# Performance work log

Hardware: AMD Instinct MI355X
Metric: run time of the kernel (lower is better)

## Reference

```python
import jax, jax.numpy as jnp
import numpy as np

N_KV, GROUP, D = 8, 4, 128
N_HEADS = N_KV * GROUP  # 32
B = 16
CONTEXT = 32768
S_CACHE = 32640  # pad = CONTEXT - B - S_CACHE = 112
NEG_INF = -10000.0


def setup_inputs() -> dict:
    key = jax.random.key(0)
    ks = jax.random.split(key, 5)
    queries = jax.random.normal(ks[0], (N_HEADS, B, D), jnp.float32)
    keys = jax.random.normal(ks[1], (N_KV, B, D), jnp.float32)
    key_t_caches = jax.random.normal(ks[2], (N_KV, D, S_CACHE), jnp.float32)
    values = jax.random.normal(ks[3], (N_KV, B, D), jnp.float32)
    value_caches = jax.random.normal(ks[4], (N_KV, S_CACHE, D), jnp.float32)
    # causal + padding mask bias: cache positions fully visible; new token j
    # sees new tokens 0..j; padded tail (and future new tokens) masked.
    pos = jnp.arange(CONTEXT)  # [context]
    new_idx = pos - S_CACHE
    qidx = jnp.arange(B)[:, None]  # [B,1]
    valid = (pos[None, :] < S_CACHE) | ((new_idx[None, :] >= 0) & (new_idx[None, :] <= qidx) & (new_idx[None, :] < B))
    attn_bias = jnp.where(valid, 0.0, NEG_INF).astype(jnp.float32)  # [B, context]
    kq_scale = jnp.float32(1.0 / np.sqrt(D))
    return {"queries": queries, "keys": keys, "key_t_caches": key_t_caches,
            "values": values, "value_caches": value_caches,
            "attn_bias": attn_bias, "kq_scale": kq_scale}


def reference(queries, keys, key_t_caches, values, value_caches, attn_bias, kq_scale):
    n_kv, d, s_cache = key_t_caches.shape
    n_heads, b, _ = queries.shape
    group = n_heads // n_kv
    context = attn_bias.shape[-1]
    pad = context - b - s_cache

    scaled_keys = keys * kq_scale                      # [n_kv, B, D]
    scaled_values = jnp.maximum(values, NEG_INF)       # [n_kv, B, D]

    key_t = jnp.swapaxes(scaled_keys, 1, 2)            # [n_kv, D, B]
    padded_key_t = jnp.pad(key_t, ((0, 0), (0, 0), (0, pad)))
    all_keys_t = jnp.concatenate([key_t_caches, padded_key_t], axis=-1)   # [n_kv, D, context]

    padded_values = jnp.pad(scaled_values, ((0, 0), (0, pad), (0, 0)))
    all_values = jnp.concatenate([value_caches, padded_values], axis=1)   # [n_kv, context, D]

    q = queries.reshape(n_kv, group, b, d)             # grouped queries per kv head
    scores = jnp.einsum('kgbd,kdc->kgbc', q, all_keys_t) + attn_bias      # [n_kv, g, B, context]
    probs = jax.nn.softmax(scores, axis=-1)
    out = jnp.einsum('kgbc,kcd->kgbd', probs, all_values)                 # [n_kv, g, B, D]
    # torch.cat(head_outs, dim=-1): head order = kv*group + g
    out = jnp.transpose(out, (2, 0, 1, 3)).reshape(b, n_heads * d)        # [B, n_heads*D]
    return out, scaled_keys, scaled_values
```

## Files before the change

### kernel.cpp

```cpp
#include <hip/hip_runtime.h>
#include <hip/hip_bf16.h>

#define NKV 8
#define GROUP 4
#define NH 32
#define BQ 16
#define DH 128
#define SC 32640
#define CTX 32768
#define SVALID (SC + BQ)
#define NEGB (-10000.0f)
#define CH2 128
#define KST 136
#define VST 68
#define PST 72
#define SPLIT_BYTES 266240ull

typedef short bf16x4 __attribute__((ext_vector_type(4)));
typedef short bf16x8 __attribute__((ext_vector_type(8)));
typedef float f32x4 __attribute__((ext_vector_type(4)));

static __device__ __forceinline__ short f2bf(float f) {
  __hip_bfloat16 h = __float2bfloat16(f);
  short s; __builtin_memcpy(&s, &h, sizeof(s));
  return s;
}
static __device__ __forceinline__ unsigned pack2(float lo, float hi) {
  return ((unsigned)(unsigned short)f2bf(lo)) | (((unsigned)(unsigned short)f2bf(hi)) << 16);
}

__global__ __launch_bounds__(256, 2)
void attn_partial(const float* __restrict__ q,
                  const float* __restrict__ keys,
                  const float* __restrict__ ktc,
                  const float* __restrict__ values,
                  const float* __restrict__ vc,
                  const float* __restrict__ kq_scale_p,
                  float* __restrict__ ws_acc,
                  float* __restrict__ ws_ml,
                  int splen)
{
  __shared__ __align__(16) short k_sh[128 * KST];
  __shared__ __align__(16) short v_sh[2][128 * VST];
  __shared__ __align__(16) short p_sh[4][16 * PST];

  const int kv    = blockIdx.y;
  const int split = blockIdx.x;
  const int tid   = threadIdx.x;
  const int wid   = tid >> 6;
  const int lane  = tid & 63;
  const int l15   = lane & 15;
  const int l4    = lane >> 4;
  const int hg    = kv * GROUP + wid;
  const float kscale = *kq_scale_p;

  bf16x8 qb[4];
  {
    const float* qrow = q + ((size_t)hg * BQ + l15) * DH + l4 * 8;
    #pragma unroll
    for (int kk = 0; kk < 4; ++kk) {
      #pragma unroll
      for (int j = 0; j < 8; ++j) qb[kk][j] = f2bf(qrow[kk * 32 + j]);
    }
  }

  float m_run = -3.0e38f, l_run = 0.f;
  f32x4 acc[8];
  #pragma unroll
  for (int n = 0; n < 8; ++n) acc[n] = (f32x4){0.f, 0.f, 0.f, 0.f};

  const int c_begin = split * splen;
  int c_end      = c_begin + splen; if (c_end > SVALID) c_end = SVALID;
  int staged_end = c_begin + splen; if (staged_end > SC) staged_end = SC;
  const int nch  = (staged_end - c_begin) >> 7;

  float4 kregL[8], kregH[8], vreg[16];

  auto load_k = [&](int cc) {
    const float* kp = ktc + (size_t)kv * DH * SC + cc;
    #pragma unroll
    for (int p = 0; p < 8; ++p) {
      const int d = p * 16 + (tid >> 4);
      const float* row = kp + (size_t)d * SC + (tid & 15) * 4;
      kregL[p] = *reinterpret_cast<const float4*>(row);
      kregH[p] = *reinterpret_cast<const float4*>(row + 64);
    }
  };
  auto load_v = [&](int cc) {
    const float* vp = vc + ((size_t)kv * SC + cc) * DH;
    #pragma unroll
    for (int p = 0; p < 16; ++p) {
      const int c = p * 8 + (tid >> 5);
      vreg[p] = *reinterpret_cast<const float4*>(vp + (size_t)c * DH + (tid & 31) * 4);
    }
  };
  auto store_k_half = [&](float4 (&kr)[8], int h) {
    const int u  = tid & 15;
    const int r  = (tid >> 4) & 3;
    const int wv = tid >> 6;
    #pragma unroll
    for (int p = 0; p < 8; ++p) {
      float x[4] = {kr[p].x, kr[p].y, kr[p].z, kr[p].w};
      float x2[4], y[4];
      #pragma unroll
      for (int c = 0; c < 4; ++c) {
        float s = __shfl_xor(x[c ^ 1], 16);
        x2[c] = ((c ^ r) & 1) ? s : x[c];
      }
      #pragma unroll
      for (int c = 0; c < 4; ++c) {
        float s = __shfl_xor(x2[c ^ 2], 32);
        y[c] = ((c ^ r) & 2) ? s : x2[c];
      }
      bf16x4 wk;
      #pragma unroll
      for (int j = 0; j < 4; ++j) wk[j] = f2bf(y[j]);
      *reinterpret_cast<bf16x4*>(&k_sh[(h * 64 + 4 * u + r) * KST + p * 16 + 4 * wv]) = wk;
    }
  };
  auto store_v = [&]() {
    const int b5 = (tid >> 5) & 1;
    #pragma unroll
    for (int p = 0; p < 16; ++p) {
      short* vs = v_sh[p >> 3];
      const float v0 = vreg[p].x, v1 = vreg[p].y, v2 = vreg[p].z, v3 = vreg[p].w;
      const float s0 = b5 ? v0 : v2;
      const float s1 = b5 ? v1 : v3;
      const float r0 = __shfl_xor(s0, 32);
      const float r1 = __shfl_xor(s1, 32);
      const float lo0 = b5 ? r0 : v0, hi0 = b5 ? v2 : r0;
      const float lo1 = b5 ? r1 : v1, hi1 = b5 ? v3 : r1;
      const int db = 4 * (tid & 31) + 2 * b5;
      const int c0 = (p & 7) * 8 + ((tid >> 5) & ~1);
      *reinterpret_cast<unsigned*>(&vs[(db + 0) * VST + c0]) = pack2(lo0, hi0);
      *reinterpret_cast<unsigned*>(&vs[(db + 1) * VST + c0]) = pack2(lo1, hi1);
    }
  };

  auto compute_half = [&](int h) {
    f32x4 s4[4];
    #pragma unroll
    for (int t = 0; t < 4; ++t) {
      f32x4 cacc = {0.f, 0.f, 0.f, 0.f};
      #pragma unroll
      for (int kk = 0; kk < 4; ++kk) {
        const bf16x8 ka = *reinterpret_cast<const bf16x8*>(
            &k_sh[(h * 64 + t * 16 + l15) * KST + kk * 32 + l4 * 8]);
        cacc = __builtin_amdgcn_mfma_f32_16x16x32_bf16(ka, qb[kk], cacc, 0, 0, 0);
      }
      s4[t] = cacc;
    }

    float mx = s4[0][0];
    #pragma unroll
    for (int t = 0; t < 4; ++t)
      #pragma unroll
      for (int r = 0; r < 4; ++r) mx = fmaxf(mx, s4[t][r]);
    mx = fmaxf(mx, __shfl_xor(mx, 16));
    mx = fmaxf(mx, __shfl_xor(mx, 32));
    const float mnew  = fmaxf(m_run, mx);
    const float alpha = __expf(m_run - mnew);
    m_run = mnew;
    float rs = 0.f;
    #pragma unroll
    for (int t = 0; t < 4; ++t) {
      bf16x4 pw;
      #pragma unroll
      for (int r = 0; r < 4; ++r) {
        const float pex = __expf(s4[t][r] - mnew);
        rs += pex;
        pw[r] = f2bf(pex);
      }
      *reinterpret_cast<bf16x4*>(&p_sh[wid][l15 * PST + t * 16 + l4 * 4]) = pw;
    }
    rs += __shfl_xor(rs, 16);
    rs += __shfl_xor(rs, 32);
    l_run = l_run * alpha + rs;

    float al[4];
    #pragma unroll
    for (int r = 0; r < 4; ++r) al[r] = __shfl(alpha, l4 * 4 + r);
    #pragma unroll
    for (int n = 0; n < 8; ++n)
      #pragma unroll
      for (int r = 0; r < 4; ++r) acc[n][r] *= al[r];

    bf16x8 pa[2];
    #pragma unroll
    for (int k2 = 0; k2 < 2; ++k2)
      pa[k2] = *reinterpret_cast<const bf16x8*>(&p_sh[wid][l15 * PST + k2 * 32 + l4 * 8]);

    const short* vs = v_sh[h];
    #pragma unroll
    for (int n = 0; n < 8; ++n) {
      #pragma unroll
      for (int k2 = 0; k2 < 2; ++k2) {
        const int base = (n * 16 + l15) * VST + k2 * 32 + l4 * 8;
        const bf16x4 vlo = *reinterpret_cast<const bf16x4*>(&vs[base]);
        const bf16x4 vhi = *reinterpret_cast<const bf16x4*>(&vs[base + 4]);
        const bf16x8 vb = __builtin_shufflevector(vlo, vhi, 0, 1, 2, 3, 4, 5, 6, 7);
        acc[n] = __builtin_amdgcn_mfma_f32_16x16x32_bf16(pa[k2], vb, acc[n], 0, 0, 0);
      }
    }
  };

  if (nch > 0) { load_k(c_begin); load_v(c_begin); }

  for (int i = 0; i < nch; ++i) {
    __syncthreads();
    store_k_half(kregL, 0);
    store_k_half(kregH, 1);
    store_v();
    __syncthreads();
    if (i + 1 < nch) {
      load_k(c_begin + (i + 1) * CH2);
      load_v(c_begin + (i + 1) * CH2);
    }
    compute_half(0);
    compute_half(1);
  }

  if (c_end > SC) {
    f32x4 s4[4];
    #pragma unroll
    for (int t = 0; t < 4; ++t) {
      f32x4 cacc = {0.f, 0.f, 0.f, 0.f};
      const int c = t * 16 + l15;
      #pragma unroll
      for (int kk = 0; kk < 4; ++kk) {
        bf16x8 kb;
        #pragma unroll
        for (int j = 0; j < 8; ++j) {
          const int dd = kk * 32 + l4 * 8 + j;
          float kf = (c < BQ) ? keys[((size_t)kv * BQ + c) * DH + dd] * kscale : 0.f;
          kb[j] = f2bf(kf);
        }
        cacc = __builtin_amdgcn_mfma_f32_16x16x32_bf16(kb, qb[kk], cacc, 0, 0, 0);
      }
      #pragma unroll
      for (int r = 0; r < 4; ++r) {
        const int cc = t * 16 + l4 * 4 + r;
        if (cc > l15) cacc[r] += NEGB;
      }
      s4[t] = cacc;
    }

    float mx = s4[0][0];
    #pragma unroll
    for (int t = 0; t < 4; ++t)
      #pragma unroll
      for (int r = 0; r < 4; ++r) mx = fmaxf(mx, s4[t][r]);
    mx = fmaxf(mx, __shfl_xor(mx, 16));
    mx = fmaxf(mx, __shfl_xor(mx, 32));
    const float mnew  = fmaxf(m_run, mx);
    const float alpha = __expf(m_run - mnew);
    m_run = mnew;
    float rs = 0.f;
    #pragma unroll
    for (int t = 0; t < 4; ++t) {
      bf16x4 pw;
      #pragma unroll
      for (int r = 0; r < 4; ++r) {
        const float pex = __expf(s4[t][r] - mnew);
        rs += pex;
        pw[r] = f2bf(pex);
      }
      *reinterpret_cast<bf16x4*>(&p_sh[wid][l15 * PST + t * 16 + l4 * 4]) = pw;
    }
    rs += __shfl_xor(rs, 16);
    rs += __shfl_xor(rs, 32);
    l_run = l_run * alpha + rs;

    float al[4];
    #pragma unroll
    for (int r = 0; r < 4; ++r) al[r] = __shfl(alpha, l4 * 4 + r);
    #pragma unroll
    for (int n = 0; n < 8; ++n)
      #pragma unroll
      for (int r = 0; r < 4; ++r) acc[n][r] *= al[r];

    bf16x8 pa2[2];
    #pragma unroll
    for (int k2 = 0; k2 < 2; ++k2)
      pa2[k2] = *reinterpret_cast<const bf16x8*>(&p_sh[wid][l15 * PST + k2 * 32 + l4 * 8]);

    #pragma unroll
    for (int n = 0; n < 8; ++n) {
      const int dcol = n * 16 + l15;
      #pragma unroll
      for (int k2 = 0; k2 < 2; ++k2) {
        bf16x8 vb;
        #pragma unroll
        for (int j = 0; j < 8; ++j) {
          const int s2 = k2 * 32 + l4 * 8 + j;
          float vf = (s2 < BQ) ? fmaxf(values[((size_t)kv * BQ + s2) * DH + dcol], NEGB) : 0.f;
          vb[j] = f2bf(vf);
        }
        acc[n] = __builtin_amdgcn_mfma_f32_16x16x32_bf16(pa2[k2], vb, acc[n], 0, 0, 0);
      }
    }
  }

  #pragma unroll
  for (int n = 0; n < 8; ++n) {
    #pragma unroll
    for (int r = 0; r < 4; ++r) {
      ws_acc[(((size_t)split * NH + hg) * BQ + l4 * 4 + r) * DH + n * 16 + l15] = acc[n][r];
    }
  }
  if (lane < BQ) {
    const size_t base = (((size_t)split * NH + hg) * BQ + lane) * 2;
    ws_ml[base]     = m_run;
    ws_ml[base + 1] = l_run;
  }
}

__global__ void attn_reduce(const float* __restrict__ ws_acc,
                            const float* __restrict__ ws_ml,
                            float* __restrict__ out, int nsplit)
{
  const int hg = blockIdx.x;
  const int b  = blockIdx.y;
  const int d  = threadIdx.x;
  float M = -3.0e38f, L = 0.f, v = 0.f;
  for (int s = 0; s < nsplit; ++s) {
    const size_t rbase = ((size_t)s * NH + hg) * BQ + b;
    const float ms = ws_ml[rbase * 2];
    const float ls = ws_ml[rbase * 2 + 1];
    const float mn = fmaxf(M, ms);
    const float c0 = __expf(M - mn);
    const float c1 = __expf(ms - mn);
    v = v * c0 + c1 * ws_acc[rbase * DH + d];
    L = L * c0 + c1 * ls;
    M = mn;
  }
  out[((size_t)b * NH + hg) * DH + d] = v / L;
}

__global__ void scale_kv(const float* __restrict__ keys,
                         const float* __restrict__ values,
                         const float* __restrict__ kq_scale_p,
                         float* __restrict__ out_sk,
                         float* __restrict__ out_sv)
{
  const int i = blockIdx.x * 256 + threadIdx.x;
  const float s = *kq_scale_p;
  if (i < NKV * BQ * DH) {
    out_sk[i] = keys[i] * s;
    out_sv[i] = fmaxf(values[i], NEGB);
  }
}

extern "C" void kernel_launch(void* const* d_in, const int* in_sizes, int n_in,
                              void* d_out, int out_size, void* d_ws, size_t ws_size,
                              hipStream_t stream)
{
  const float* q    = (const float*)d_in[0];
  const float* keys = (const float*)d_in[1];
  const float* ktc  = (const float*)d_in[2];
  const float* vals = (const float*)d_in[3];
  const float* vc   = (const float*)d_in[4];
  const float* kqs  = (const float*)d_in[6];

  float* out    = (float*)d_out;
  float* out_sk = out + BQ * NH * DH;
  float* out_sv = out_sk + NKV * BQ * DH;

  int nsplit = 64;
  while (nsplit > 1 && (size_t)nsplit * SPLIT_BYTES > ws_size) nsplit >>= 1;
  const int splen = CTX / nsplit;

  float* ws_acc = (float*)d_ws;
  float* ws_ml  = ws_acc + (size_t)nsplit * NH * BQ * DH;

  hipLaunchKernelGGL(attn_partial, dim3(nsplit, NKV), dim3(256), 0, stream,
                     q, keys, ktc, vals, vc, kqs, ws_acc, ws_ml, splen);
  hipLaunchKernelGGL(attn_reduce, dim3(NH, BQ), dim3(DH), 0, stream,
                     ws_acc, ws_ml, out, nsplit);
  hipLaunchKernelGGL(scale_kv, dim3((NKV * BQ * DH + 255) / 256), dim3(256), 0, stream,
                     keys, vals, kqs, out_sk, out_sv);
}
```

Before: 98.59 us.

## Pack K cache to bf16 in registers and load two chunks per K fetch

K tiles are converted to packed bf16 pairs right after the global load, which halves the register footprint per chunk. That freed space is used to prefetch two 128-column K chunks at once, every other iteration. The LDS transpose now shuffles packed 32-bit words with one xor-16 exchange instead of two float shuffle stages, so fewer shuffles and conversions run per store. In exchange, K loads become bursty (double size every second phase), and the 64-register K buffer can raise register pressure and lower occupancy.

Measured after the change: 93.98 us. 1.05x faster.

```diff
diff --git a/kernel.cpp b/kernel.cpp
--- a/kernel.cpp
+++ b/kernel.cpp
@@ -10,7 +10,6 @@
 #define CTX 32768
 #define SVALID (SC + BQ)
 #define NEGB (-10000.0f)
-#define CH2 128
 #define KST 136
 #define VST 68
 #define PST 72
@@ -72,18 +71,31 @@
   const int c_begin = split * splen;
   int c_end      = c_begin + splen; if (c_end > SVALID) c_end = SVALID;
   int staged_end = c_begin + splen; if (staged_end > SC) staged_end = SC;
-  const int nch  = (staged_end - c_begin) >> 7;
-
-  float4 kregL[8], kregH[8], vreg[16];
-
-  auto load_k = [&](int cc) {
+  const int nph  = (staged_end - c_begin) >> 7;
+
+  unsigned kpk[8][8];
+  float4 vreg[16];
+
+  auto load_k = [&](int cc, bool two) {
     const float* kp = ktc + (size_t)kv * DH * SC + cc;
     #pragma unroll
     for (int p = 0; p < 8; ++p) {
       const int d = p * 16 + (tid >> 4);
       const float* row = kp + (size_t)d * SC + (tid & 15) * 4;
-      kregL[p] = *reinterpret_cast<const float4*>(row);
-      kregH[p] = *reinterpret_cast<const float4*>(row + 64);
+      #pragma unroll
+      for (int s = 0; s < 2; ++s) {
+        const float4 f = *reinterpret_cast<const float4*>(row + s * 64);
+        kpk[p][s * 2]     = pack2(f.x, f.y);
+        kpk[p][s * 2 + 1] = pack2(f.z, f.w);
+      }
+      if (two) {
+        #pragma unroll
+        for (int s = 2; s < 4; ++s) {
+          const float4 f = *reinterpret_cast<const float4*>(row + s * 64);
+          kpk[p][s * 2]     = pack2(f.x, f.y);
+          kpk[p][s * 2 + 1] = pack2(f.z, f.w);
+        }
+      }
     }
   };
   auto load_v = [&](int cc) {
@@ -94,28 +106,30 @@
       vreg[p] = *reinterpret_cast<const float4*>(vp + (size_t)c * DH + (tid & 31) * 4);
     }
   };
-  auto store_k_half = [&](float4 (&kr)[8], int h) {
-    const int u  = tid & 15;
-    const int r  = (tid >> 4) & 3;
-    const int wv = tid >> 6;
+
+  auto store_k_seg = [&](int s, int h) {
+    const int g  = (tid >> 4) & 1;
+    const int dp = ((tid >> 4) & ~1);
+    const int cb = h * 64 + 4 * (tid & 15);
     #pragma unroll
     for (int p = 0; p < 8; ++p) {
-      float x[4] = {kr[p].x, kr[p].y, kr[p].z, kr[p].w};
-      float x2[4], y[4];
-      #pragma unroll
-      for (int c = 0; c < 4; ++c) {
-        float s = __shfl_xor(x[c ^ 1], 16);
-        x2[c] = ((c ^ r) & 1) ? s : x[c];
-      }
-      #pragma unroll
-      for (int c = 0; c < 4; ++c) {
-        float s = __shfl_xor(x2[c ^ 2], 32);
-        y[c] = ((c ^ r) & 2) ? s : x2[c];
-      }
-      bf16x4 wk;
-      #pragma unroll
-      for (int j = 0; j < 4; ++j) wk[j] = f2bf(y[j]);
-      *reinterpret_cast<bf16x4*>(&k_sh[(h * 64 + 4 * u + r) * KST + p * 16 + 4 * wv]) = wk;
+      const unsigned A  = kpk[p][s * 2];
+      const unsigned B  = kpk[p][s * 2 + 1];
+      const unsigned tA = (unsigned)__shfl_xor((int)A, 16);
+      const unsigned tB = (unsigned)__shfl_xor((int)B, 16);
+      unsigned u0, u1; int c0;
+      if (g == 0) {
+        u0 = (A & 0xFFFFu) | (tA << 16);
+        u1 = (A >> 16)     | (tA & 0xFFFF0000u);
+        c0 = cb;
+      } else {
+        u0 = (tB & 0xFFFFu) | (B << 16);
+        u1 = (tB >> 16)     | (B & 0xFFFF0000u);
+        c0 = cb + 2;
+      }
+      const int dd = p * 16 + dp;
+      *reinterpret_cast<unsigned*>(&k_sh[(c0    ) * KST + dd]) = u0;
+      *reinterpret_cast<unsigned*>(&k_sh[(c0 + 1) * KST + dd]) = u1;
     }
   };
   auto store_v = [&]() {
@@ -204,18 +218,16 @@
     }
   };
 
-  if (nch > 0) { load_k(c_begin); load_v(c_begin); }
-
-  for (int i = 0; i < nch; ++i) {
+  if (nph > 0) { load_k(c_begin, nph > 1); load_v(c_begin); }
+
+  for (int j = 0; j < nph; ++j) {
     __syncthreads();
-    store_k_half(kregL, 0);
-    store_k_half(kregH, 1);
+    if ((j & 1) == 0) { store_k_seg(0, 0); store_k_seg(1, 1); }
+    else              { store_k_seg(2, 0); store_k_seg(3, 1); }
     store_v();
     __syncthreads();
-    if (i + 1 < nch) {
-      load_k(c_begin + (i + 1) * CH2);
-      load_v(c_begin + (i + 1) * CH2);
-    }
+    if (j + 1 < nph) load_v(c_begin + (j + 1) * 128);
+    if ((j & 1) && j + 1 < nph) load_k(c_begin + (j + 1) * 128, j + 2 < nph);
     compute_half(0);
     compute_half(1);
   }
```
